# Performance work log

Measured on AMD Instinct MI355X. Metric: run time of the kernel, lower is better.

The kernel has to match this reference:

```python
import jax, jax.numpy as jnp
import numpy as np

N_ITEMS = 200000
N_USERS = 100000
N_INTER = 2000000  # ragged user->item interactions, avg ~20 per user
GCN, HID, TOW = 64, 256, 128


def setup_inputs() -> dict:
    key = jax.random.key(0)
    ks = jax.random.split(key, 9)
    s = 0.05
    return {
        "item_feat": jax.random.normal(ks[0], (N_ITEMS, 2), jnp.float32),
        "gcn_item_emb": jax.random.normal(ks[1], (N_ITEMS, GCN), jnp.float32),
        "gcn_user_emb": jax.random.normal(ks[2], (N_USERS, GCN), jnp.float32),
        "Wi1": jax.random.normal(ks[3], (GCN + 2, HID), jnp.float32) * s,
        "bi1": jnp.zeros((HID,), jnp.float32),
        "Wi2": jax.random.normal(ks[4], (HID, TOW), jnp.float32) * s,
        "bi2": jnp.zeros((TOW,), jnp.float32),
        "Wu1": jax.random.normal(ks[5], (GCN + TOW, HID), jnp.float32) * s,
        "bu1": jnp.zeros((HID,), jnp.float32),
        "Wu2": jax.random.normal(ks[6], (HID, TOW), jnp.float32) * s,
        "bu2": jnp.zeros((TOW,), jnp.float32),
        "item_idx": jax.random.randint(ks[7], (N_INTER,), 0, N_ITEMS),
        "seg_ids": jnp.sort(jax.random.randint(ks[8], (N_INTER,), 0, N_USERS)),
        "users": jnp.arange(N_USERS),
    }


def _l2norm(x, eps=1e-12):
    # matches torch F.normalize: x / max(||x||_2, eps)
    n = jnp.sqrt(jnp.sum(x * x, axis=-1, keepdims=True))
    return x / jnp.maximum(n, eps)


def reference(item_feat, gcn_item_emb, gcn_user_emb,
              Wi1, bi1, Wi2, bi2, Wu1, bu1, Wu2, bu2,
              item_idx, seg_ids, users):
    # encode_items: concat -> MLP -> L2 normalize
    x = jnp.concatenate([item_feat, gcn_item_emb], axis=1)          # [N_items, 66]
    item_emb = _l2norm(jax.nn.relu(x @ Wi1 + bi1) @ Wi2 + bi2)       # [N_items, TOW]

    # encode_users: ragged gather + per-user mean (segment mean)
    nu = gcn_user_emb.shape[0]
    hist_sum = jax.ops.segment_sum(item_emb[item_idx], seg_ids, num_segments=nu)
    counts = jax.ops.segment_sum(jnp.ones((seg_ids.shape[0],), item_emb.dtype),
                                 seg_ids, num_segments=nu)
    hist = hist_sum / jnp.maximum(counts, 1.0)[:, None]             # [N_users, TOW]

    fused = jnp.concatenate([gcn_user_emb[users], hist[users]], axis=1)  # [N_users, 192]
    user_emb = _l2norm(jax.nn.relu(fused @ Wu1 + bu1) @ Wu2 + bu2)   # [N_users, TOW]
    return user_emb
```

## Files before the change

### kernel.cpp

```cpp
#include <hip/hip_runtime.h>
#include <hip/hip_bf16.h>
#include <cstdint>
#include <cstddef>

#define NITEMS 200000
#define NUSERS 100000
#define NINTER 2000000

typedef __attribute__((ext_vector_type(8))) short bf16x8;
typedef __attribute__((ext_vector_type(4))) float f32x4;

__device__ __forceinline__ unsigned short f2bf(float f) {
    union { float f; unsigned u; } v; v.f = f;
    unsigned r = v.u + 0x7fffu + ((v.u >> 16) & 1u);
    return (unsigned short)(r >> 16);
}
__device__ __forceinline__ float bf2f(unsigned short h) {
    union { unsigned u; float f; } v; v.u = ((unsigned)h) << 16;
    return v.f;
}
__device__ __forceinline__ unsigned pack2(float a, float b) {
    return (unsigned)f2bf(a) | ((unsigned)f2bf(b) << 16);
}

__global__ void preconv_kernel(const float* __restrict__ Wi1, const float* __restrict__ Wi2,
                               const float* __restrict__ Wu1, const float* __restrict__ Wu2,
                               unsigned short* __restrict__ W1t, unsigned short* __restrict__ W2t,
                               unsigned short* __restrict__ W1ut, unsigned short* __restrict__ W2ut)
{
    int t = blockIdx.x * 256 + threadIdx.x;
    if (t < 256 * 96) {
        int n = t / 96, k = t % 96;
        W1t[t] = (k < 66) ? f2bf(Wi1[k * 256 + n]) : (unsigned short)0;
        return;
    }
    t -= 256 * 96;
    if (t < 128 * 256) {
        int n = t / 256, k = t % 256;
        W2t[t] = f2bf(Wi2[k * 128 + n]);
        return;
    }
    t -= 128 * 256;
    if (t < 256 * 192) {
        int n = t / 192, k = t % 192;
        W1ut[t] = f2bf(Wu1[k * 256 + n]);
        return;
    }
    t -= 256 * 192;
    if (t < 128 * 256) {
        int n = t / 256, k = t % 256;
        W2ut[t] = f2bf(Wu2[k * 128 + n]);
    }
}

#define HSI 264
#define XS  104
#define XSU 200

__global__ __launch_bounds__(256, 2)
void item_mfma_kernel(const float* __restrict__ item_feat,
                      const float* __restrict__ gcn_item,
                      const unsigned short* __restrict__ W1t,
                      const unsigned short* __restrict__ W2t,
                      const float* __restrict__ bi1, const float* __restrict__ bi2,
                      unsigned short* __restrict__ item_emb)
{
    __shared__ unsigned short Xs[64 * XS];
    __shared__ unsigned short Hs[64 * HSI];
    __shared__ float ssq[64][4];

    const int t  = threadIdx.x;
    const int w  = t >> 6;
    const int l  = t & 63;
    const int lo = l & 15;
    const int hi = l >> 4;

    bf16x8 w1f[4][3];
    #pragma unroll
    for (int mt = 0; mt < 4; ++mt)
        #pragma unroll
        for (int kt = 0; kt < 3; ++kt)
            w1f[mt][kt] = *(const bf16x8*)(W1t + (64 * w + mt * 16 + lo) * 96 + kt * 32 + hi * 8);
    bf16x8 w2f[2][8];
    #pragma unroll
    for (int ct = 0; ct < 2; ++ct)
        #pragma unroll
        for (int kt = 0; kt < 8; ++kt)
            w2f[ct][kt] = *(const bf16x8*)(W2t + (32 * w + ct * 16 + lo) * 256 + kt * 32 + hi * 8);
    f32x4 b1v[4];
    #pragma unroll
    for (int mt = 0; mt < 4; ++mt) b1v[mt] = *(const f32x4*)(bi1 + 64 * w + mt * 16 + 4 * hi);
    f32x4 b2v[2];
    #pragma unroll
    for (int ct = 0; ct < 2; ++ct) b2v[ct] = *(const f32x4*)(bi2 + 32 * w + ct * 16 + 4 * hi);

    if (t < 64) {
        unsigned* z = (unsigned*)((char*)Xs + t * (XS * 2) + 132);
        #pragma unroll
        for (int k = 0; k < 15; ++k) z[k] = 0u;
    }

    for (int tile = blockIdx.x; tile < NITEMS / 64; tile += gridDim.x) {
        const size_t i0 = (size_t)tile * 64;

        {
            const int row = t >> 2, q = t & 3;
            const float4* g = (const float4*)(gcn_item + (i0 + row) * 64 + q * 16);
            unsigned* dst = (unsigned*)((char*)Xs + row * (XS * 2) + 4 + q * 32);
            #pragma unroll
            for (int k = 0; k < 4; ++k) {
                float4 v = g[k];
                dst[2 * k]     = pack2(v.x, v.y);
                dst[2 * k + 1] = pack2(v.z, v.w);
            }
            if (q == 0) {
                float2 f = *(const float2*)(item_feat + (i0 + row) * 2);
                *(unsigned*)((char*)Xs + row * (XS * 2)) = pack2(f.x, f.y);
            }
        }
        __syncthreads();

        f32x4 acc1[4][4];
        #pragma unroll
        for (int mt = 0; mt < 4; ++mt)
            #pragma unroll
            for (int nt = 0; nt < 4; ++nt)
                acc1[mt][nt] = (f32x4)(0.0f);
        #pragma unroll
        for (int nt = 0; nt < 4; ++nt)
            #pragma unroll
            for (int kt = 0; kt < 3; ++kt) {
                bf16x8 b = *(const bf16x8*)((char*)Xs + (nt * 16 + lo) * (XS * 2) + kt * 64 + hi * 16);
                #pragma unroll
                for (int mt = 0; mt < 4; ++mt)
                    acc1[mt][nt] = __builtin_amdgcn_mfma_f32_16x16x32_bf16(w1f[mt][kt], b, acc1[mt][nt], 0, 0, 0);
            }

        #pragma unroll
        for (int mt = 0; mt < 4; ++mt)
            #pragma unroll
            for (int nt = 0; nt < 4; ++nt) {
                float v0 = fmaxf(acc1[mt][nt][0] + b1v[mt][0], 0.0f);
                float v1 = fmaxf(acc1[mt][nt][1] + b1v[mt][1], 0.0f);
                float v2 = fmaxf(acc1[mt][nt][2] + b1v[mt][2], 0.0f);
                float v3 = fmaxf(acc1[mt][nt][3] + b1v[mt][3], 0.0f);
                uint2 pk = make_uint2(pack2(v0, v1), pack2(v2, v3));
                *(uint2*)((char*)Hs + (nt * 16 + lo) * (HSI * 2) + (64 * w + mt * 16 + 4 * hi) * 2) = pk;
            }
        __syncthreads();

        f32x4 acc2[4][2];
        #pragma unroll
        for (int nt = 0; nt < 4; ++nt) { acc2[nt][0] = (f32x4)(0.0f); acc2[nt][1] = (f32x4)(0.0f); }
        #pragma unroll
        for (int nt = 0; nt < 4; ++nt)
            #pragma unroll
            for (int kt = 0; kt < 8; ++kt) {
                bf16x8 b = *(const bf16x8*)((char*)Hs + (nt * 16 + lo) * (HSI * 2) + kt * 64 + hi * 16);
                #pragma unroll
                for (int ct = 0; ct < 2; ++ct)
                    acc2[nt][ct] = __builtin_amdgcn_mfma_f32_16x16x32_bf16(w2f[ct][kt], b, acc2[nt][ct], 0, 0, 0);
            }

        #pragma unroll
        for (int nt = 0; nt < 4; ++nt) {
            float p = 0.0f;
            #pragma unroll
            for (int ct = 0; ct < 2; ++ct)
                #pragma unroll
                for (int r = 0; r < 4; ++r) {
                    float v = acc2[nt][ct][r] + b2v[ct][r];
                    acc2[nt][ct][r] = v;
                    p = fmaf(v, v, p);
                }
            p += __shfl_xor(p, 16);
            p += __shfl_xor(p, 32);
            if (hi == 0) ssq[nt * 16 + lo][w] = p;
        }
        __syncthreads();

        #pragma unroll
        for (int nt = 0; nt < 4; ++nt) {
            float4 s4 = *(const float4*)&ssq[nt * 16 + lo][0];
            float sc = 1.0f / fmaxf(sqrtf(s4.x + s4.y + s4.z + s4.w), 1e-12f);
            #pragma unroll
            for (int ct = 0; ct < 2; ++ct) {
                uint2 pk = make_uint2(pack2(acc2[nt][ct][0] * sc, acc2[nt][ct][1] * sc),
                                      pack2(acc2[nt][ct][2] * sc, acc2[nt][ct][3] * sc));
                *(uint2*)(item_emb + (i0 + nt * 16 + lo) * 128 + 32 * w + ct * 16 + 4 * hi) = pk;
            }
        }
    }
}

__global__ void seg_bounds_kernel(const int* __restrict__ seg, int* __restrict__ start)
{
    int u = blockIdx.x * 256 + threadIdx.x;
    if (u > NUSERS) return;
    int lo = 0, hi = NINTER;
    while (lo < hi) {
        int m = (lo + hi) >> 1;
        if (seg[m] < u) lo = m + 1; else hi = m;
    }
    start[u] = lo;
}

__global__ __launch_bounds__(256)
void seg_mean_kernel(const int* __restrict__ item_idx,
                     const int* __restrict__ start,
                     const unsigned short* __restrict__ item_emb,
                     unsigned short* __restrict__ hist)
{
    int gid  = blockIdx.x * 256 + threadIdx.x;
    int wave = gid >> 6;
    int lane = gid & 63;
    if (wave >= NUSERS) return;

    int s = start[wave], e = start[wave + 1];
    int n = e - s;
    float a0 = 0.0f, a1 = 0.0f;

    if (n > 0) {
        const int elast = e - 1;
        int i0 = item_idx[s];
        int i1 = item_idx[min(s + 1, elast)];
        int i2 = item_idx[min(s + 2, elast)];
        int i3 = item_idx[min(s + 3, elast)];
        for (int r = s; r < e; r += 4) {
            const int j0 = i0, j1 = i1, j2 = i2, j3 = i3;
            int rn = r + 4;
            if (rn < e) {
                i0 = item_idx[rn];
                i1 = item_idx[min(rn + 1, elast)];
                i2 = item_idx[min(rn + 2, elast)];
                i3 = item_idx[min(rn + 3, elast)];
            }
            unsigned v0 = *(const unsigned*)(item_emb + (size_t)j0 * 128 + lane * 2);
            unsigned v1 = *(const unsigned*)(item_emb + (size_t)j1 * 128 + lane * 2);
            unsigned v2 = *(const unsigned*)(item_emb + (size_t)j2 * 128 + lane * 2);
            unsigned v3 = *(const unsigned*)(item_emb + (size_t)j3 * 128 + lane * 2);
            const float m1 = (r + 1 < e) ? 1.0f : 0.0f;
            const float m2 = (r + 2 < e) ? 1.0f : 0.0f;
            const float m3 = (r + 3 < e) ? 1.0f : 0.0f;
            a0 += bf2f((unsigned short)(v0 & 0xffffu));
            a1 += bf2f((unsigned short)(v0 >> 16));
            a0 = fmaf(m1, bf2f((unsigned short)(v1 & 0xffffu)), a0);
            a1 = fmaf(m1, bf2f((unsigned short)(v1 >> 16)), a1);
            a0 = fmaf(m2, bf2f((unsigned short)(v2 & 0xffffu)), a0);
            a1 = fmaf(m2, bf2f((unsigned short)(v2 >> 16)), a1);
            a0 = fmaf(m3, bf2f((unsigned short)(v3 & 0xffffu)), a0);
            a1 = fmaf(m3, bf2f((unsigned short)(v3 >> 16)), a1);
        }
    }
    float inv = 1.0f / fmaxf((float)n, 1.0f);
    unsigned outv = pack2(a0 * inv, a1 * inv);
    *(unsigned*)(hist + (size_t)wave * 128 + lane * 2) = outv;
}

__global__ __launch_bounds__(256, 2)
void user_mfma_kernel(const float* __restrict__ gcn_user,
                      const unsigned short* __restrict__ hist,
                      const unsigned short* __restrict__ W1ut,
                      const unsigned short* __restrict__ W2ut,
                      const float* __restrict__ bu1, const float* __restrict__ bu2,
                      const int* __restrict__ users,
                      float* __restrict__ out)
{
    __shared__ unsigned short Xs[64 * XSU];
    __shared__ unsigned short Hs[64 * HSI];
    __shared__ float ssq[64][4];

    const int t  = threadIdx.x;
    const int w  = t >> 6;
    const int l  = t & 63;
    const int lo = l & 15;
    const int hi = l >> 4;
    const int NT = (NUSERS + 63) / 64;

    bf16x8 w1f[4][6];
    #pragma unroll
    for (int mt = 0; mt < 4; ++mt)
        #pragma unroll
        for (int kt = 0; kt < 6; ++kt)
            w1f[mt][kt] = *(const bf16x8*)(W1ut + (64 * w + mt * 16 + lo) * 192 + kt * 32 + hi * 8);
    f32x4 b1v[4];
    #pragma unroll
    for (int mt = 0; mt < 4; ++mt) b1v[mt] = *(const f32x4*)(bu1 + 64 * w + mt * 16 + 4 * hi);
    f32x4 b2v[2];
    #pragma unroll
    for (int ct = 0; ct < 2; ++ct) b2v[ct] = *(const f32x4*)(bu2 + 32 * w + ct * 16 + 4 * hi);

    for (int tile = blockIdx.x; tile < NT; tile += gridDim.x) {
        const int r0 = tile * 64;

        {
            const int row = t >> 2, q = t & 3;
            int rr = r0 + row;
            int u = users[rr < NUSERS ? rr : (NUSERS - 1)];
            const float4* g = (const float4*)(gcn_user + (size_t)u * 64 + q * 16);
            unsigned* dst = (unsigned*)((char*)Xs + row * (XSU * 2) + q * 32);
            #pragma unroll
            for (int k = 0; k < 4; ++k) {
                float4 v = g[k];
                dst[2 * k]     = pack2(v.x, v.y);
                dst[2 * k + 1] = pack2(v.z, v.w);
            }
            const uint4* hp = (const uint4*)(hist + (size_t)u * 128 + q * 32);
            uint4* hd = (uint4*)((char*)Xs + row * (XSU * 2) + 128 + q * 64);
            #pragma unroll
            for (int k = 0; k < 4; ++k) hd[k] = hp[k];
        }
        __syncthreads();

        f32x4 acc1[4][4];
        #pragma unroll
        for (int mt = 0; mt < 4; ++mt)
            #pragma unroll
            for (int nt = 0; nt < 4; ++nt)
                acc1[mt][nt] = (f32x4)(0.0f);
        #pragma unroll
        for (int nt = 0; nt < 4; ++nt)
            #pragma unroll
            for (int kt = 0; kt < 6; ++kt) {
                bf16x8 b = *(const bf16x8*)((char*)Xs + (nt * 16 + lo) * (XSU * 2) + kt * 64 + hi * 16);
                #pragma unroll
                for (int mt = 0; mt < 4; ++mt)
                    acc1[mt][nt] = __builtin_amdgcn_mfma_f32_16x16x32_bf16(w1f[mt][kt], b, acc1[mt][nt], 0, 0, 0);
            }

        #pragma unroll
        for (int mt = 0; mt < 4; ++mt)
            #pragma unroll
            for (int nt = 0; nt < 4; ++nt) {
                float v0 = fmaxf(acc1[mt][nt][0] + b1v[mt][0], 0.0f);
                float v1 = fmaxf(acc1[mt][nt][1] + b1v[mt][1], 0.0f);
                float v2 = fmaxf(acc1[mt][nt][2] + b1v[mt][2], 0.0f);
                float v3 = fmaxf(acc1[mt][nt][3] + b1v[mt][3], 0.0f);
                uint2 pk = make_uint2(pack2(v0, v1), pack2(v2, v3));
                *(uint2*)((char*)Hs + (nt * 16 + lo) * (HSI * 2) + (64 * w + mt * 16 + 4 * hi) * 2) = pk;
            }

        bf16x8 w2f[2][8];
        #pragma unroll
        for (int ct = 0; ct < 2; ++ct)
            #pragma unroll
            for (int kt = 0; kt < 8; ++kt)
                w2f[ct][kt] = *(const bf16x8*)(W2ut + (32 * w + ct * 16 + lo) * 256 + kt * 32 + hi * 8);
        __syncthreads();

        f32x4 acc2[4][2];
        #pragma unroll
        for (int nt = 0; nt < 4; ++nt) { acc2[nt][0] = (f32x4)(0.0f); acc2[nt][1] = (f32x4)(0.0f); }
        #pragma unroll
        for (int nt = 0; nt < 4; ++nt)
            #pragma unroll
            for (int kt = 0; kt < 8; ++kt) {
                bf16x8 b = *(const bf16x8*)((char*)Hs + (nt * 16 + lo) * (HSI * 2) + kt * 64 + hi * 16);
                #pragma unroll
                for (int ct = 0; ct < 2; ++ct)
                    acc2[nt][ct] = __builtin_amdgcn_mfma_f32_16x16x32_bf16(w2f[ct][kt], b, acc2[nt][ct], 0, 0, 0);
            }

        #pragma unroll
        for (int nt = 0; nt < 4; ++nt) {
            float p = 0.0f;
            #pragma unroll
            for (int ct = 0; ct < 2; ++ct)
                #pragma unroll
                for (int r = 0; r < 4; ++r) {
                    float v = acc2[nt][ct][r] + b2v[ct][r];
                    acc2[nt][ct][r] = v;
                    p = fmaf(v, v, p);
                }
            p += __shfl_xor(p, 16);
            p += __shfl_xor(p, 32);
            if (hi == 0) ssq[nt * 16 + lo][w] = p;
        }
        __syncthreads();

        #pragma unroll
        for (int nt = 0; nt < 4; ++nt) {
            int row = r0 + nt * 16 + lo;
            float4 s4 = *(const float4*)&ssq[nt * 16 + lo][0];
            float sc = 1.0f / fmaxf(sqrtf(s4.x + s4.y + s4.z + s4.w), 1e-12f);
            if (row < NUSERS) {
                #pragma unroll
                for (int ct = 0; ct < 2; ++ct) {
                    float4 st = make_float4(acc2[nt][ct][0] * sc, acc2[nt][ct][1] * sc,
                                            acc2[nt][ct][2] * sc, acc2[nt][ct][3] * sc);
                    *(float4*)(out + (size_t)row * 128 + 32 * w + ct * 16 + 4 * hi) = st;
                }
            }
        }
    }
}

extern "C" void kernel_launch(void* const* d_in, const int* in_sizes, int n_in,
                              void* d_out, int out_size, void* d_ws, size_t ws_size,
                              hipStream_t stream)
{
    const float* item_feat = (const float*)d_in[0];
    const float* gcn_item  = (const float*)d_in[1];
    const float* gcn_user  = (const float*)d_in[2];
    const float* Wi1 = (const float*)d_in[3];
    const float* bi1 = (const float*)d_in[4];
    const float* Wi2 = (const float*)d_in[5];
    const float* bi2 = (const float*)d_in[6];
    const float* Wu1 = (const float*)d_in[7];
    const float* bu1 = (const float*)d_in[8];
    const float* Wu2 = (const float*)d_in[9];
    const float* bu2 = (const float*)d_in[10];
    const int* item_idx = (const int*)d_in[11];
    const int* seg_ids  = (const int*)d_in[12];
    const int* users    = (const int*)d_in[13];
    float* out = (float*)d_out;

    char* ws = (char*)d_ws;
    unsigned short* item_emb = (unsigned short*)ws;
    unsigned short* hist = (unsigned short*)(ws + (size_t)NITEMS * 256);
    size_t off = (size_t)NITEMS * 256 + (size_t)NUSERS * 256;
    int* start = (int*)(ws + off);
    off += ((size_t)(NUSERS + 1) * 4 + 255) & ~(size_t)255;
    unsigned short* W1t  = (unsigned short*)(ws + off); off += 256 * 96 * 2;
    unsigned short* W2t  = (unsigned short*)(ws + off); off += 128 * 256 * 2;
    unsigned short* W1ut = (unsigned short*)(ws + off); off += 256 * 192 * 2;
    unsigned short* W2ut = (unsigned short*)(ws + off);

    hipLaunchKernelGGL(preconv_kernel, dim3(544), dim3(256), 0, stream,
                       Wi1, Wi2, Wu1, Wu2, W1t, W2t, W1ut, W2ut);

    hipLaunchKernelGGL(seg_bounds_kernel, dim3((NUSERS + 1 + 255) / 256), dim3(256), 0, stream,
                       seg_ids, start);

    hipLaunchKernelGGL(item_mfma_kernel, dim3(512), dim3(256), 0, stream,
                       item_feat, gcn_item, W1t, W2t, bi1, bi2, item_emb);

    hipLaunchKernelGGL(seg_mean_kernel, dim3(NUSERS / 4), dim3(256), 0, stream,
                       item_idx, start, item_emb, hist);

    hipLaunchKernelGGL(user_mfma_kernel, dim3(512), dim3(256), 0, stream,
                       gcn_user, hist, W1ut, W2ut, bu1, bu2, users, out);
}
```

Before: 331.6 us.

## Stream weight fragments per k-step and merge prep and segment-bound kernels

The item and user MLP kernels no longer keep all weight fragments and biases in registers for the whole persistent loop. Each k-step now reloads its weight fragments from global memory (L1/L2-resident), and biases are loaded just before the epilogue. This lowers VGPR pressure and may allow higher occupancy, at the cost of repeated global loads on every tile. Separately, the weight-conversion kernel and the segment-bounds binary search are fused into one launch to save a kernel launch.

After: 315.3 us. 4.9% less time.

```diff
diff --git a/kernel.cpp b/kernel.cpp
--- a/kernel.cpp
+++ b/kernel.cpp
@@ -23,10 +23,12 @@
     return (unsigned)f2bf(a) | ((unsigned)f2bf(b) << 16);
 }
 
-__global__ void preconv_kernel(const float* __restrict__ Wi1, const float* __restrict__ Wi2,
-                               const float* __restrict__ Wu1, const float* __restrict__ Wu2,
-                               unsigned short* __restrict__ W1t, unsigned short* __restrict__ W2t,
-                               unsigned short* __restrict__ W1ut, unsigned short* __restrict__ W2ut)
+__global__ void prep_kernel(const float* __restrict__ Wi1, const float* __restrict__ Wi2,
+                            const float* __restrict__ Wu1, const float* __restrict__ Wu2,
+                            const int* __restrict__ seg,
+                            unsigned short* __restrict__ W1t, unsigned short* __restrict__ W2t,
+                            unsigned short* __restrict__ W1ut, unsigned short* __restrict__ W2ut,
+                            int* __restrict__ start)
 {
     int t = blockIdx.x * 256 + threadIdx.x;
     if (t < 256 * 96) {
@@ -50,6 +52,16 @@
     if (t < 128 * 256) {
         int n = t / 256, k = t % 256;
         W2ut[t] = f2bf(Wu2[k * 128 + n]);
+        return;
+    }
+    t -= 128 * 256;
+    if (t <= NUSERS) {
+        int lo = 0, hi = NINTER;
+        while (lo < hi) {
+            int m = (lo + hi) >> 1;
+            if (seg[m] < t) lo = m + 1; else hi = m;
+        }
+        start[t] = lo;
     }
 }
 
@@ -75,25 +87,6 @@
     const int lo = l & 15;
     const int hi = l >> 4;
 
-    bf16x8 w1f[4][3];
-    #pragma unroll
-    for (int mt = 0; mt < 4; ++mt)
-        #pragma unroll
-        for (int kt = 0; kt < 3; ++kt)
-            w1f[mt][kt] = *(const bf16x8*)(W1t + (64 * w + mt * 16 + lo) * 96 + kt * 32 + hi * 8);
-    bf16x8 w2f[2][8];
-    #pragma unroll
-    for (int ct = 0; ct < 2; ++ct)
-        #pragma unroll
-        for (int kt = 0; kt < 8; ++kt)
-            w2f[ct][kt] = *(const bf16x8*)(W2t + (32 * w + ct * 16 + lo) * 256 + kt * 32 + hi * 8);
-    f32x4 b1v[4];
-    #pragma unroll
-    for (int mt = 0; mt < 4; ++mt) b1v[mt] = *(const f32x4*)(bi1 + 64 * w + mt * 16 + 4 * hi);
-    f32x4 b2v[2];
-    #pragma unroll
-    for (int ct = 0; ct < 2; ++ct) b2v[ct] = *(const f32x4*)(bi2 + 32 * w + ct * 16 + 4 * hi);
-
     if (t < 64) {
         unsigned* z = (unsigned*)((char*)Xs + t * (XS * 2) + 132);
         #pragma unroll
@@ -127,55 +120,71 @@
             for (int nt = 0; nt < 4; ++nt)
                 acc1[mt][nt] = (f32x4)(0.0f);
         #pragma unroll
-        for (int nt = 0; nt < 4; ++nt)
-            #pragma unroll
-            for (int kt = 0; kt < 3; ++kt) {
+        for (int kt = 0; kt < 3; ++kt) {
+            bf16x8 wf[4];
+            #pragma unroll
+            for (int mt = 0; mt < 4; ++mt)
+                wf[mt] = *(const bf16x8*)(W1t + (64 * w + mt * 16 + lo) * 96 + kt * 32 + hi * 8);
+            #pragma unroll
+            for (int nt = 0; nt < 4; ++nt) {
                 bf16x8 b = *(const bf16x8*)((char*)Xs + (nt * 16 + lo) * (XS * 2) + kt * 64 + hi * 16);
                 #pragma unroll
                 for (int mt = 0; mt < 4; ++mt)
-                    acc1[mt][nt] = __builtin_amdgcn_mfma_f32_16x16x32_bf16(w1f[mt][kt], b, acc1[mt][nt], 0, 0, 0);
-            }
-
-        #pragma unroll
-        for (int mt = 0; mt < 4; ++mt)
-            #pragma unroll
-            for (int nt = 0; nt < 4; ++nt) {
-                float v0 = fmaxf(acc1[mt][nt][0] + b1v[mt][0], 0.0f);
-                float v1 = fmaxf(acc1[mt][nt][1] + b1v[mt][1], 0.0f);
-                float v2 = fmaxf(acc1[mt][nt][2] + b1v[mt][2], 0.0f);
-                float v3 = fmaxf(acc1[mt][nt][3] + b1v[mt][3], 0.0f);
+                    acc1[mt][nt] = __builtin_amdgcn_mfma_f32_16x16x32_bf16(wf[mt], b, acc1[mt][nt], 0, 0, 0);
+            }
+        }
+
+        #pragma unroll
+        for (int mt = 0; mt < 4; ++mt) {
+            f32x4 b1 = *(const f32x4*)(bi1 + 64 * w + mt * 16 + 4 * hi);
+            #pragma unroll
+            for (int nt = 0; nt < 4; ++nt) {
+                float v0 = fmaxf(acc1[mt][nt][0] + b1[0], 0.0f);
+                float v1 = fmaxf(acc1[mt][nt][1] + b1[1], 0.0f);
+                float v2 = fmaxf(acc1[mt][nt][2] + b1[2], 0.0f);
+                float v3 = fmaxf(acc1[mt][nt][3] + b1[3], 0.0f);
                 uint2 pk = make_uint2(pack2(v0, v1), pack2(v2, v3));
                 *(uint2*)((char*)Hs + (nt * 16 + lo) * (HSI * 2) + (64 * w + mt * 16 + 4 * hi) * 2) = pk;
             }
+        }
         __syncthreads();
 
         f32x4 acc2[4][2];
         #pragma unroll
         for (int nt = 0; nt < 4; ++nt) { acc2[nt][0] = (f32x4)(0.0f); acc2[nt][1] = (f32x4)(0.0f); }
         #pragma unroll
-        for (int nt = 0; nt < 4; ++nt)
-            #pragma unroll
-            for (int kt = 0; kt < 8; ++kt) {
+        for (int kt = 0; kt < 8; ++kt) {
+            bf16x8 wf[2];
+            #pragma unroll
+            for (int ct = 0; ct < 2; ++ct)
+                wf[ct] = *(const bf16x8*)(W2t + (32 * w + ct * 16 + lo) * 256 + kt * 32 + hi * 8);
+            #pragma unroll
+            for (int nt = 0; nt < 4; ++nt) {
                 bf16x8 b = *(const bf16x8*)((char*)Hs + (nt * 16 + lo) * (HSI * 2) + kt * 64 + hi * 16);
                 #pragma unroll
                 for (int ct = 0; ct < 2; ++ct)
-                    acc2[nt][ct] = __builtin_amdgcn_mfma_f32_16x16x32_bf16(w2f[ct][kt], b, acc2[nt][ct], 0, 0, 0);
-            }
-
-        #pragma unroll
-        for (int nt = 0; nt < 4; ++nt) {
-            float p = 0.0f;
-            #pragma unroll
-            for (int ct = 0; ct < 2; ++ct)
+                    acc2[nt][ct] = __builtin_amdgcn_mfma_f32_16x16x32_bf16(wf[ct], b, acc2[nt][ct], 0, 0, 0);
+            }
+        }
+
+        {
+            f32x4 b2a = *(const f32x4*)(bi2 + 32 * w + 4 * hi);
+            f32x4 b2b = *(const f32x4*)(bi2 + 32 * w + 16 + 4 * hi);
+            #pragma unroll
+            for (int nt = 0; nt < 4; ++nt) {
+                float p = 0.0f;
                 #pragma unroll
                 for (int r = 0; r < 4; ++r) {
-                    float v = acc2[nt][ct][r] + b2v[ct][r];
-                    acc2[nt][ct][r] = v;
-                    p = fmaf(v, v, p);
+                    float v0 = acc2[nt][0][r] + b2a[r];
+                    float v1 = acc2[nt][1][r] + b2b[r];
+                    acc2[nt][0][r] = v0;
+                    acc2[nt][1][r] = v1;
+                    p = fmaf(v0, v0, fmaf(v1, v1, p));
                 }
-            p += __shfl_xor(p, 16);
-            p += __shfl_xor(p, 32);
-            if (hi == 0) ssq[nt * 16 + lo][w] = p;
+                p += __shfl_xor(p, 16);
+                p += __shfl_xor(p, 32);
+                if (hi == 0) ssq[nt * 16 + lo][w] = p;
+            }
         }
         __syncthreads();
 
@@ -191,18 +200,6 @@
             }
         }
     }
-}
-
-__global__ void seg_bounds_kernel(const int* __restrict__ seg, int* __restrict__ start)
-{
-    int u = blockIdx.x * 256 + threadIdx.x;
-    if (u > NUSERS) return;
-    int lo = 0, hi = NINTER;
-    while (lo < hi) {
-        int m = (lo + hi) >> 1;
-        if (seg[m] < u) lo = m + 1; else hi = m;
-    }
-    start[u] = lo;
 }
 
 __global__ __launch_bounds__(256)
@@ -277,19 +274,6 @@
     const int hi = l >> 4;
     const int NT = (NUSERS + 63) / 64;
 
-    bf16x8 w1f[4][6];
-    #pragma unroll
-    for (int mt = 0; mt < 4; ++mt)
-        #pragma unroll
-        for (int kt = 0; kt < 6; ++kt)
-            w1f[mt][kt] = *(const bf16x8*)(W1ut + (64 * w + mt * 16 + lo) * 192 + kt * 32 + hi * 8);
-    f32x4 b1v[4];
-    #pragma unroll
-    for (int mt = 0; mt < 4; ++mt) b1v[mt] = *(const f32x4*)(bu1 + 64 * w + mt * 16 + 4 * hi);
-    f32x4 b2v[2];
-    #pragma unroll
-    for (int ct = 0; ct < 2; ++ct) b2v[ct] = *(const f32x4*)(bu2 + 32 * w + ct * 16 + 4 * hi);
-
     for (int tile = blockIdx.x; tile < NT; tile += gridDim.x) {
         const int r0 = tile * 64;
 
@@ -319,62 +303,71 @@
             for (int nt = 0; nt < 4; ++nt)
                 acc1[mt][nt] = (f32x4)(0.0f);
         #pragma unroll
-        for (int nt = 0; nt < 4; ++nt)
-            #pragma unroll
-            for (int kt = 0; kt < 6; ++kt) {
+        for (int kt = 0; kt < 6; ++kt) {
+            bf16x8 wf[4];
+            #pragma unroll
+            for (int mt = 0; mt < 4; ++mt)
+                wf[mt] = *(const bf16x8*)(W1ut + (64 * w + mt * 16 + lo) * 192 + kt * 32 + hi * 8);
+            #pragma unroll
+            for (int nt = 0; nt < 4; ++nt) {
                 bf16x8 b = *(const bf16x8*)((char*)Xs + (nt * 16 + lo) * (XSU * 2) + kt * 64 + hi * 16);
                 #pragma unroll
                 for (int mt = 0; mt < 4; ++mt)
-                    acc1[mt][nt] = __builtin_amdgcn_mfma_f32_16x16x32_bf16(w1f[mt][kt], b, acc1[mt][nt], 0, 0, 0);
-            }
-
-        #pragma unroll
-        for (int mt = 0; mt < 4; ++mt)
-            #pragma unroll
-            for (int nt = 0; nt < 4; ++nt) {
-                float v0 = fmaxf(acc1[mt][nt][0] + b1v[mt][0], 0.0f);
-                float v1 = fmaxf(acc1[mt][nt][1] + b1v[mt][1], 0.0f);
-                float v2 = fmaxf(acc1[mt][nt][2] + b1v[mt][2], 0.0f);
-                float v3 = fmaxf(acc1[mt][nt][3] + b1v[mt][3], 0.0f);
+                    acc1[mt][nt] = __builtin_amdgcn_mfma_f32_16x16x32_bf16(wf[mt], b, acc1[mt][nt], 0, 0, 0);
+            }
+        }
+
+        #pragma unroll
+        for (int mt = 0; mt < 4; ++mt) {
+            f32x4 b1 = *(const f32x4*)(bu1 + 64 * w + mt * 16 + 4 * hi);
+            #pragma unroll
+            for (int nt = 0; nt < 4; ++nt) {
+                float v0 = fmaxf(acc1[mt][nt][0] + b1[0], 0.0f);
+                float v1 = fmaxf(acc1[mt][nt][1] + b1[1], 0.0f);
+                float v2 = fmaxf(acc1[mt][nt][2] + b1[2], 0.0f);
+                float v3 = fmaxf(acc1[mt][nt][3] + b1[3], 0.0f);
                 uint2 pk = make_uint2(pack2(v0, v1), pack2(v2, v3));
                 *(uint2*)((char*)Hs + (nt * 16 + lo) * (HSI * 2) + (64 * w + mt * 16 + 4 * hi) * 2) = pk;
             }
-
-        bf16x8 w2f[2][8];
-        #pragma unroll
-        for (int ct = 0; ct < 2; ++ct)
-            #pragma unroll
-            for (int kt = 0; kt < 8; ++kt)
-                w2f[ct][kt] = *(const bf16x8*)(W2ut + (32 * w + ct * 16 + lo) * 256 + kt * 32 + hi * 8);
+        }
         __syncthreads();
 
         f32x4 acc2[4][2];
         #pragma unroll
         for (int nt = 0; nt < 4; ++nt) { acc2[nt][0] = (f32x4)(0.0f); acc2[nt][1] = (f32x4)(0.0f); }
         #pragma unroll
-        for (int nt = 0; nt < 4; ++nt)
-            #pragma unroll
-            for (int kt = 0; kt < 8; ++kt) {
+        for (int kt = 0; kt < 8; ++kt) {
+            bf16x8 wf[2];
+            #pragma unroll
+            for (int ct = 0; ct < 2; ++ct)
+                wf[ct] = *(const bf16x8*)(W2ut + (32 * w + ct * 16 + lo) * 256 + kt * 32 + hi * 8);
+            #pragma unroll
+            for (int nt = 0; nt < 4; ++nt) {
                 bf16x8 b = *(const bf16x8*)((char*)Hs + (nt * 16 + lo) * (HSI * 2) + kt * 64 + hi * 16);
                 #pragma unroll
                 for (int ct = 0; ct < 2; ++ct)
-                    acc2[nt][ct] = __builtin_amdgcn_mfma_f32_16x16x32_bf16(w2f[ct][kt], b, acc2[nt][ct], 0, 0, 0);
-            }
-
-        #pragma unroll
-        for (int nt = 0; nt < 4; ++nt) {
-            float p = 0.0f;
-            #pragma unroll
-            for (int ct = 0; ct < 2; ++ct)
+                    acc2[nt][ct] = __builtin_amdgcn_mfma_f32_16x16x32_bf16(wf[ct], b, acc2[nt][ct], 0, 0, 0);
+            }
+        }
+
+        {
+            f32x4 b2a = *(const f32x4*)(bu2 + 32 * w + 4 * hi);
+            f32x4 b2b = *(const f32x4*)(bu2 + 32 * w + 16 + 4 * hi);
+            #pragma unroll
+            for (int nt = 0; nt < 4; ++nt) {
+                float p = 0.0f;
                 #pragma unroll
                 for (int r = 0; r < 4; ++r) {
-                    float v = acc2[nt][ct][r] + b2v[ct][r];
-                    acc2[nt][ct][r] = v;
-                    p = fmaf(v, v, p);
+                    float v0 = acc2[nt][0][r] + b2a[r];
+                    float v1 = acc2[nt][1][r] + b2b[r];
+                    acc2[nt][0][r] = v0;
+                    acc2[nt][1][r] = v1;
+                    p = fmaf(v0, v0, fmaf(v1, v1, p));
                 }
-            p += __shfl_xor(p, 16);
-            p += __shfl_xor(p, 32);
-            if (hi == 0) ssq[nt * 16 + lo][w] = p;
+                p += __shfl_xor(p, 16);
+                p += __shfl_xor(p, 32);
+                if (hi == 0) ssq[nt * 16 + lo][w] = p;
+            }
         }
         __syncthreads();
 
@@ -426,11 +419,8 @@
     unsigned short* W1ut = (unsigned short*)(ws + off); off += 256 * 192 * 2;
     unsigned short* W2ut = (unsigned short*)(ws + off);
 
-    hipLaunchKernelGGL(preconv_kernel, dim3(544), dim3(256), 0, stream,
-                       Wi1, Wi2, Wu1, Wu2, W1t, W2t, W1ut, W2ut);
-
-    hipLaunchKernelGGL(seg_bounds_kernel, dim3((NUSERS + 1 + 255) / 256), dim3(256), 0, stream,
-                       seg_ids, start);
+    hipLaunchKernelGGL(prep_kernel, dim3((139264 + NUSERS + 1 + 255) / 256), dim3(256), 0, stream,
+                       Wi1, Wi2, Wu1, Wu2, seg_ids, W1t, W2t, W1ut, W2ut, start);
 
     hipLaunchKernelGGL(item_mfma_kernel, dim3(512), dim3(256), 0, stream,
                        item_feat, gcn_item, W1t, W2t, bi1, bi2, item_emb);
```
